# Performance work log

Measured on AMD Instinct MI355X. Metric: run time of the kernel, lower is better.

## Reference

```python
import jax, jax.numpy as jnp
import numpy as np

B, N, IN_F, OUT_F, H = 4, 2048, 128, 128, 4
D = OUT_F // H  # head_dim = 32
NEG_SLOPE = 0.2


def setup_inputs() -> dict:
    key = jax.random.key(0)
    k1, k2, k3, k4, k5 = jax.random.split(key, 5)
    x = jax.random.normal(k1, (B, N, IN_F), dtype=jnp.float32)
    adj = jax.random.randint(k2, (N, N), 0, 2, dtype=jnp.int32)
    adj = adj.at[jnp.arange(N), jnp.arange(N)].set(1)  # self-loops
    # xavier-uniform-like init
    lim_w = float(np.sqrt(6.0 / (IN_F + OUT_F)))
    W = jax.random.uniform(k3, (OUT_F, IN_F), minval=-lim_w, maxval=lim_w, dtype=jnp.float32)
    lim_a = float(np.sqrt(6.0 / (H + D)))
    a_src = jax.random.uniform(k4, (H, D), minval=-lim_a, maxval=lim_a, dtype=jnp.float32)
    a_dst = jax.random.uniform(k5, (H, D), minval=-lim_a, maxval=lim_a, dtype=jnp.float32)
    return {"x": x, "adj": adj, "W": W, "a_src": a_src, "a_dst": a_dst}


def reference(x, adj, W, a_src, a_dst):
    Bx, Nx, _ = x.shape
    # linear projection: (B,N,out) -> (B,N,H,D)
    h = jnp.einsum('bni,oi->bno', x, W).reshape(Bx, Nx, H, D)
    e_src = jnp.einsum('bnhd,hd->bnh', h, a_src)  # (B,N,H)
    e_dst = jnp.einsum('bnhd,hd->bnh', h, a_dst)  # (B,N,H)
    # scores: (B,N_src,H,N_dst)
    scores = jax.nn.leaky_relu(
        e_src[:, :, :, None] + e_dst.transpose(0, 2, 1)[:, None, :, :],
        negative_slope=NEG_SLOPE,
    )
    mask = adj[None, :, None, :]  # (1,N,1,N)
    scores = jnp.where(mask == 0, -jnp.inf, scores)
    attn = jax.nn.softmax(scores, axis=-1)  # (B,N,H,N); dropout is identity at eval
    out = jnp.einsum('bnhm,bmhd->bnhd', attn, h)  # (B,N,H,D)
    return out.reshape(Bx, Nx, H * D)
```

## Files before the change

### kernel.cpp

```cpp
#include <hip/hip_runtime.h>
#include <math.h>

#define BB 4
#define NN 2048
#define FF 128
#define HH 4
#define DD 32
#define NEG_SLOPE 0.2f
#define LOG2E 1.4426950408889634f

typedef __attribute__((ext_vector_type(8))) short short8;
typedef __attribute__((ext_vector_type(4))) float floatx4;
typedef __attribute__((ext_vector_type(2))) float floatx2;

__device__ __forceinline__ float exp2_fast(float x) {
#if __has_builtin(__builtin_amdgcn_exp2f)
    return __builtin_amdgcn_exp2f(x);
#else
    return exp2f(x);
#endif
}

__device__ __forceinline__ int bit_mask(unsigned int w, int bit) {
#if __has_builtin(__builtin_amdgcn_sbfe)
    return __builtin_amdgcn_sbfe((int)w, bit, 1);
#else
    return ((int)(w << (31 - bit))) >> 31;
#endif
}

__device__ __forceinline__ unsigned short to_bf16(float f) {
    unsigned int ui = __float_as_uint(f);
    ui += 0x7FFFu + ((ui >> 16) & 1u);
    return (unsigned short)(ui >> 16);
}

__global__ __launch_bounds__(256) void k_prep(const float* __restrict__ x,
                                              const float* __restrict__ W,
                                              const float* __restrict__ a_src,
                                              const float* __restrict__ a_dst,
                                              const int* __restrict__ adj,
                                              unsigned short* __restrict__ ht,
                                              float* __restrict__ es_t,
                                              float* __restrict__ ed_t,
                                              unsigned int* __restrict__ bits) {
    __shared__ float xs[16][FF];
    __shared__ float wt[32][132];
    __shared__ float as_s[FF], ad_s[FF];
    __shared__ unsigned short tile2[16][136];
    int t = threadIdx.x;

    if (blockIdx.x >= 512) {
        int idx = (blockIdx.x - 512) * 256 + t;
        int n = idx >> 6, w = idx & 63;
        const int4* base = (const int4*)(adj + (size_t)n * NN + w * 32);
        unsigned int word = 0;
#pragma unroll
        for (int q = 0; q < 8; ++q) {
            int4 a = base[q];
            word |= ((unsigned int)(a.x & 1)) << (q * 4 + 0);
            word |= ((unsigned int)(a.y & 1)) << (q * 4 + 1);
            word |= ((unsigned int)(a.z & 1)) << (q * 4 + 2);
            word |= ((unsigned int)(a.w & 1)) << (q * 4 + 3);
        }
        bits[idx] = word;
        return;
    }

    long rows0 = (long)blockIdx.x * 16;
    if (t < FF) { as_s[t] = a_src[t]; ad_s[t] = a_dst[t]; }
#pragma unroll
    for (int k = 0; k < 2; ++k) {
        int q = t + k * 256;
        int r = q >> 5, c4 = q & 31;
        float4 v = ((const float4*)(x + (rows0 + r) * FF))[c4];
        *(float4*)&xs[r][c4 * 4] = v;
    }
    int og = t & 31, rg = t >> 5;
    float acc[2][4];
#pragma unroll
    for (int a = 0; a < 2; ++a)
#pragma unroll
        for (int c = 0; c < 4; ++c) acc[a][c] = 0.f;

    int wo = t & 127, wg = t >> 7;
    for (int i0 = 0; i0 < FF; i0 += 32) {
        __syncthreads();
#pragma unroll
        for (int u = 0; u < 4; ++u) {
            float4 v = *(const float4*)(W + (long)wo * FF + i0 + wg * 16 + u * 4);
            wt[wg * 16 + u * 4 + 0][wo] = v.x;
            wt[wg * 16 + u * 4 + 1][wo] = v.y;
            wt[wg * 16 + u * 4 + 2][wo] = v.z;
            wt[wg * 16 + u * 4 + 3][wo] = v.w;
        }
        __syncthreads();
#pragma unroll
        for (int i = 0; i < 32; ++i) {
            float4 w4 = *(const float4*)&wt[i][og * 4];
            float x0 = xs[rg * 2 + 0][i0 + i];
            float x1 = xs[rg * 2 + 1][i0 + i];
            acc[0][0] += x0 * w4.x; acc[0][1] += x0 * w4.y;
            acc[0][2] += x0 * w4.z; acc[0][3] += x0 * w4.w;
            acc[1][0] += x1 * w4.x; acc[1][1] += x1 * w4.y;
            acc[1][2] += x1 * w4.z; acc[1][3] += x1 * w4.w;
        }
    }

    int head = og >> 3;
    int b = (int)(rows0 >> 11);
    int m_block = (int)(rows0 & 2047);
    float es0 = 0.f, ed0 = 0.f, es1 = 0.f, ed1 = 0.f;
#pragma unroll
    for (int c = 0; c < 4; ++c) {
        int col = og * 4 + c;
        es0 += acc[0][c] * as_s[col]; ed0 += acc[0][c] * ad_s[col];
        es1 += acc[1][c] * as_s[col]; ed1 += acc[1][c] * ad_s[col];
    }
#pragma unroll
    for (int k = 1; k < 8; k <<= 1) {
        es0 += __shfl_xor(es0, k); ed0 += __shfl_xor(ed0, k);
        es1 += __shfl_xor(es1, k); ed1 += __shfl_xor(ed1, k);
    }
    if ((og & 7) == 0) {
        size_t eb = (size_t)(b * HH + head) * NN + m_block + rg * 2;
        es_t[eb]     = es0 * LOG2E; ed_t[eb]     = ed0 * LOG2E;
        es_t[eb + 1] = es1 * LOG2E; ed_t[eb + 1] = ed1 * LOG2E;
    }

#pragma unroll
    for (int a = 0; a < 2; ++a)
#pragma unroll
        for (int c = 0; c < 4; ++c)
            tile2[rg * 2 + a][og * 4 + c] = to_bf16(acc[a][c]);
    __syncthreads();
    {
        int cg = t >> 1, half = t & 1;
        int d = cg & 31, hd = cg >> 5;
        unsigned short tmp[8];
#pragma unroll
        for (int j = 0; j < 8; ++j) tmp[j] = tile2[half * 8 + j][cg];
        unsigned short* op = ht + ((size_t)(b * HH + hd) * DD + d) * NN + m_block + half * 8;
        *(int4*)op = *(const int4*)tmp;
    }
}

#define HTS 2056
__global__ __launch_bounds__(1024) void k_attn(
        const unsigned short* __restrict__ ht,
        const unsigned int* __restrict__ bits,
        const float* __restrict__ es_t,
        const float* __restrict__ ed_t,
        float* __restrict__ out) {
    __shared__ unsigned short hb[DD * HTS];
    __shared__ float ep[NN * 2];
    int t = threadIdx.x;
    int n0 = blockIdx.x * 128;
    int bh = blockIdx.y;
    int b = bh >> 2, head = bh & 3;

    int wid = t >> 6, lane = t & 63;
    int q = lane >> 4, r = lane & 15;
    int qo = q * 8;
    int half = wid >> 3, wsub = wid & 7;
    int n_l = wsub * 16 + r;

    {
        float2 v = ((const float2*)(ed_t + (size_t)bh * NN))[t];
        float4 o;
        o.x = exp2_fast(v.x); o.y = exp2_fast(NEG_SLOPE * v.x);
        o.z = exp2_fast(v.y); o.w = exp2_fast(NEG_SLOPE * v.y);
        ((float4*)ep)[t] = o;
    }
    {
        const unsigned short* htp = ht + (size_t)bh * DD * NN;
#pragma unroll
        for (int k = 0; k < 8; ++k) {
            int qq = t + k * 1024;
            int d = qq >> 8, cm = qq & 255;
            int4 v = *(const int4*)(htp + (size_t)d * NN + cm * 8);
            *(int4*)&hb[d * HTS + cm * 8] = v;
        }
    }
    int4 bw[8];
    {
        const int4* bp = (const int4*)(bits + (size_t)(n0 + n_l) * 64 + half * 32);
#pragma unroll
        for (int g = 0; g < 8; ++g) bw[g] = bp[g];
    }
    float esv = es_t[(size_t)bh * NN + n0 + n_l];
    floatx2 es2 = {exp2_fast(esv), exp2_fast(NEG_SLOPE * esv)};
    __syncthreads();

    floatx4 acc0 = {0.f, 0.f, 0.f, 0.f};
    floatx4 acc1 = {0.f, 0.f, 0.f, 0.f};
    floatx4 accd = {0.f, 0.f, 0.f, 0.f};
    union { short8 s8; int i[4]; } ones;
    ones.i[0] = 0x3F803F80; ones.i[1] = 0x3F803F80;
    ones.i[2] = 0x3F803F80; ones.i[3] = 0x3F803F80;

    const float* eph = ep + half * 2048;
    const unsigned short* hrow0 = &hb[r * HTS + half * 1024 + qo];
    const unsigned short* hrow1 = hrow0 + 16 * HTS;

#pragma unroll
    for (int g = 0; g < 8; ++g) {
#pragma unroll
        for (int c = 0; c < 4; ++c) {
            unsigned int word = (unsigned int)((&bw[g].x)[c]);
            int mb = (g * 4 + c) * 32;
            unsigned int wq = word >> qo;
            const float* pbase = eph + (mb + qo) * 2;
            union { short8 s8; int i[4]; } af;
#pragma unroll
            for (int jp = 0; jp < 4; ++jp) {
                float4 d2 = *(const float4*)(pbase + jp * 4);
                floatx2 p0 = es2 * (floatx2){d2.x, d2.y};
                floatx2 p1 = es2 * (floatx2){d2.z, d2.w};
                float w0 = fmaxf(p0.x, p0.y);
                float w1 = fmaxf(p1.x, p1.y);
                int m0 = bit_mask(wq, 2 * jp);
                int m1 = bit_mask(wq, 2 * jp + 1);
                w0 = __uint_as_float(__float_as_uint(w0) & (unsigned int)m0);
                w1 = __uint_as_float(__float_as_uint(w1) & (unsigned int)m1);
                af.i[jp] = __builtin_amdgcn_perm(__float_as_uint(w1),
                                                 __float_as_uint(w0),
                                                 0x07060302u);
            }
            short8 b0 = *(const short8*)(hrow0 + mb);
            short8 b1 = *(const short8*)(hrow1 + mb);
            acc0 = __builtin_amdgcn_mfma_f32_16x16x32_bf16(af.s8, b0, acc0, 0, 0, 0);
            acc1 = __builtin_amdgcn_mfma_f32_16x16x32_bf16(af.s8, b1, acc1, 0, 0, 0);
            accd = __builtin_amdgcn_mfma_f32_16x16x32_bf16(af.s8, ones.s8, accd, 0, 0, 0);
        }
    }

    __syncthreads();
    float* scr = (float*)hb;
    if (wid >= 8) {
        int base = ((wid - 8) * 64 + lane) * 12;
        *(floatx4*)&scr[base + 0] = acc0;
        *(floatx4*)&scr[base + 4] = acc1;
        *(floatx4*)&scr[base + 8] = accd;
    }
    __syncthreads();
    if (wid < 8) {
        int base = (wid * 64 + lane) * 12;
        floatx4 p0 = *(const floatx4*)&scr[base + 0];
        floatx4 p1 = *(const floatx4*)&scr[base + 4];
        floatx4 pd = *(const floatx4*)&scr[base + 8];
#pragma unroll
        for (int k = 0; k < 4; ++k) {
            acc0[k] += p0[k]; acc1[k] += p1[k]; accd[k] += pd[k];
        }
#pragma unroll
        for (int reg = 0; reg < 4; ++reg) {
            int nrow = n0 + wsub * 16 + q * 4 + reg;
            float inv = 1.0f / accd[reg];
            float* op = out + ((size_t)(b * NN + nrow)) * FF + head * DD;
            op[r]      = acc0[reg] * inv;
            op[16 + r] = acc1[reg] * inv;
        }
    }
}

extern "C" void kernel_launch(void* const* d_in, const int* in_sizes, int n_in,
                              void* d_out, int out_size, void* d_ws, size_t ws_size,
                              hipStream_t stream) {
    const float* x     = (const float*)d_in[0];
    const int*   adj   = (const int*)d_in[1];
    const float* W     = (const float*)d_in[2];
    const float* a_src = (const float*)d_in[3];
    const float* a_dst = (const float*)d_in[4];
    float* out = (float*)d_out;

    float* es_t = (float*)d_ws;
    float* ed_t = es_t + (size_t)BB * HH * NN;
    unsigned int* bits = (unsigned int*)(ed_t + (size_t)BB * HH * NN);
    unsigned short* ht = (unsigned short*)(bits + (size_t)NN * (NN / 32));

    hipLaunchKernelGGL(k_prep, dim3(1024), dim3(256), 0, stream,
                       x, W, a_src, a_dst, adj, ht, es_t, ed_t, bits);
    hipLaunchKernelGGL(k_attn, dim3(NN / 128, BB * HH), dim3(1024), 0, stream,
                       ht, bits, es_t, ed_t, out);
}
```

Measured before the change: 102.5 us.

## Restructure prep GEMM tiling and halve attention block with packed bf16 exp tables

The prep kernel drops to 128 threads per block, each computing a 4x4 output tile with float4 dot products over a row-major W tile, and the bitmask blocks are regridded to match. The attention kernel uses 64-row blocks of 512 threads and stages h in two 1024-column halves to cut shared memory, which should raise occupancy. It also stores the destination exp pair as packed bf16 in one uint instead of two floats. The cost is an extra barrier-separated load phase and reduced precision in the exponent factors.

```diff
diff --git a/kernel.cpp b/kernel.cpp
--- a/kernel.cpp
+++ b/kernel.cpp
@@ -35,7 +35,13 @@
     return (unsigned short)(ui >> 16);
 }
 
-__global__ __launch_bounds__(256) void k_prep(const float* __restrict__ x,
+__device__ __forceinline__ unsigned int pack_pair(float e) {
+    unsigned int p = to_bf16(exp2_fast(e));
+    unsigned int n = to_bf16(exp2_fast(NEG_SLOPE * e));
+    return (p << 16) | n;
+}
+
+__global__ __launch_bounds__(128) void k_prep(const float* __restrict__ x,
                                               const float* __restrict__ W,
                                               const float* __restrict__ a_src,
                                               const float* __restrict__ a_dst,
@@ -44,14 +50,14 @@
                                               float* __restrict__ es_t,
                                               float* __restrict__ ed_t,
                                               unsigned int* __restrict__ bits) {
-    __shared__ float xs[16][FF];
-    __shared__ float wt[32][132];
+    __shared__ float xs[16][132];
+    __shared__ float wb[128][36];
     __shared__ float as_s[FF], ad_s[FF];
     __shared__ unsigned short tile2[16][136];
     int t = threadIdx.x;
 
     if (blockIdx.x >= 512) {
-        int idx = (blockIdx.x - 512) * 256 + t;
+        int idx = (blockIdx.x - 512) * 128 + t;
         int n = idx >> 6, w = idx & 63;
         const int4* base = (const int4*)(adj + (size_t)n * NN + w * 32);
         unsigned int word = 0;
@@ -68,129 +74,137 @@
     }
 
     long rows0 = (long)blockIdx.x * 16;
-    if (t < FF) { as_s[t] = a_src[t]; ad_s[t] = a_dst[t]; }
-#pragma unroll
-    for (int k = 0; k < 2; ++k) {
-        int q = t + k * 256;
-        int r = q >> 5, c4 = q & 31;
-        float4 v = ((const float4*)(x + (rows0 + r) * FF))[c4];
-        *(float4*)&xs[r][c4 * 4] = v;
+    as_s[t] = a_src[t]; ad_s[t] = a_dst[t];
+#pragma unroll
+    for (int k = 0; k < 4; ++k) {
+        int idx = t + k * 128;
+        int r = idx >> 5, f4 = idx & 31;
+        float4 v = ((const float4*)(x + (rows0 + r) * FF))[f4];
+        *(float4*)&xs[r][f4 * 4] = v;
     }
     int og = t & 31, rg = t >> 5;
-    float acc[2][4];
-#pragma unroll
-    for (int a = 0; a < 2; ++a)
+    float acc[4][4];
+#pragma unroll
+    for (int a = 0; a < 4; ++a)
 #pragma unroll
         for (int c = 0; c < 4; ++c) acc[a][c] = 0.f;
 
-    int wo = t & 127, wg = t >> 7;
-    for (int i0 = 0; i0 < FF; i0 += 32) {
+    for (int c4 = 0; c4 < 4; ++c4) {
         __syncthreads();
 #pragma unroll
-        for (int u = 0; u < 4; ++u) {
-            float4 v = *(const float4*)(W + (long)wo * FF + i0 + wg * 16 + u * 4);
-            wt[wg * 16 + u * 4 + 0][wo] = v.x;
-            wt[wg * 16 + u * 4 + 1][wo] = v.y;
-            wt[wg * 16 + u * 4 + 2][wo] = v.z;
-            wt[wg * 16 + u * 4 + 3][wo] = v.w;
+        for (int k = 0; k < 8; ++k) {
+            int idx = t + k * 128;
+            int wr = idx >> 3, f4 = idx & 7;
+            float4 v = *(const float4*)(W + (long)wr * FF + c4 * 32 + f4 * 4);
+            *(float4*)&wb[wr][f4 * 4] = v;
         }
         __syncthreads();
 #pragma unroll
-        for (int i = 0; i < 32; ++i) {
-            float4 w4 = *(const float4*)&wt[i][og * 4];
-            float x0 = xs[rg * 2 + 0][i0 + i];
-            float x1 = xs[rg * 2 + 1][i0 + i];
-            acc[0][0] += x0 * w4.x; acc[0][1] += x0 * w4.y;
-            acc[0][2] += x0 * w4.z; acc[0][3] += x0 * w4.w;
-            acc[1][0] += x1 * w4.x; acc[1][1] += x1 * w4.y;
-            acc[1][2] += x1 * w4.z; acc[1][3] += x1 * w4.w;
+        for (int ii = 0; ii < 8; ++ii) {
+            int i = ii * 4;
+            float4 xv[4], wv[4];
+#pragma unroll
+            for (int a = 0; a < 4; ++a)
+                xv[a] = *(const float4*)&xs[rg * 4 + a][c4 * 32 + i];
+#pragma unroll
+            for (int c = 0; c < 4; ++c)
+                wv[c] = *(const float4*)&wb[og * 4 + c][i];
+#pragma unroll
+            for (int a = 0; a < 4; ++a)
+#pragma unroll
+                for (int c = 0; c < 4; ++c) {
+                    acc[a][c] += xv[a].x * wv[c].x + xv[a].y * wv[c].y
+                               + xv[a].z * wv[c].z + xv[a].w * wv[c].w;
+                }
         }
     }
 
     int head = og >> 3;
     int b = (int)(rows0 >> 11);
     int m_block = (int)(rows0 & 2047);
-    float es0 = 0.f, ed0 = 0.f, es1 = 0.f, ed1 = 0.f;
-#pragma unroll
-    for (int c = 0; c < 4; ++c) {
-        int col = og * 4 + c;
-        es0 += acc[0][c] * as_s[col]; ed0 += acc[0][c] * ad_s[col];
-        es1 += acc[1][c] * as_s[col]; ed1 += acc[1][c] * ad_s[col];
+    float es[4], ed[4];
+#pragma unroll
+    for (int a = 0; a < 4; ++a) {
+        float s = 0.f, d = 0.f;
+#pragma unroll
+        for (int c = 0; c < 4; ++c) {
+            int col = og * 4 + c;
+            s += acc[a][c] * as_s[col];
+            d += acc[a][c] * ad_s[col];
+        }
+        es[a] = s; ed[a] = d;
     }
 #pragma unroll
     for (int k = 1; k < 8; k <<= 1) {
-        es0 += __shfl_xor(es0, k); ed0 += __shfl_xor(ed0, k);
-        es1 += __shfl_xor(es1, k); ed1 += __shfl_xor(ed1, k);
+#pragma unroll
+        for (int a = 0; a < 4; ++a) {
+            es[a] += __shfl_xor(es[a], k);
+            ed[a] += __shfl_xor(ed[a], k);
+        }
     }
     if ((og & 7) == 0) {
-        size_t eb = (size_t)(b * HH + head) * NN + m_block + rg * 2;
-        es_t[eb]     = es0 * LOG2E; ed_t[eb]     = ed0 * LOG2E;
-        es_t[eb + 1] = es1 * LOG2E; ed_t[eb + 1] = ed1 * LOG2E;
-    }
-
-#pragma unroll
-    for (int a = 0; a < 2; ++a)
+        size_t eb = (size_t)(b * HH + head) * NN + m_block + rg * 4;
+#pragma unroll
+        for (int a = 0; a < 4; ++a) {
+            es_t[eb + a] = es[a] * LOG2E;
+            ed_t[eb + a] = ed[a] * LOG2E;
+        }
+    }
+
+#pragma unroll
+    for (int a = 0; a < 4; ++a)
 #pragma unroll
         for (int c = 0; c < 4; ++c)
-            tile2[rg * 2 + a][og * 4 + c] = to_bf16(acc[a][c]);
+            tile2[rg * 4 + a][og * 4 + c] = to_bf16(acc[a][c]);
     __syncthreads();
     {
-        int cg = t >> 1, half = t & 1;
-        int d = cg & 31, hd = cg >> 5;
-        unsigned short tmp[8];
-#pragma unroll
-        for (int j = 0; j < 8; ++j) tmp[j] = tile2[half * 8 + j][cg];
-        unsigned short* op = ht + ((size_t)(b * HH + hd) * DD + d) * NN + m_block + half * 8;
-        *(int4*)op = *(const int4*)tmp;
-    }
-}
-
-#define HTS 2056
-__global__ __launch_bounds__(1024) void k_attn(
+        int col = t;
+        int hd = col >> 5, d = col & 31;
+        unsigned short* op = ht + ((size_t)(b * HH + hd) * DD + d) * NN + m_block;
+#pragma unroll
+        for (int h2 = 0; h2 < 2; ++h2) {
+            unsigned short tmp[8];
+#pragma unroll
+            for (int j = 0; j < 8; ++j) tmp[j] = tile2[h2 * 8 + j][col];
+            *(int4*)(op + h2 * 8) = *(const int4*)tmp;
+        }
+    }
+}
+
+#define HBS 1032
+__global__ __launch_bounds__(512) void k_attn(
         const unsigned short* __restrict__ ht,
         const unsigned int* __restrict__ bits,
         const float* __restrict__ es_t,
         const float* __restrict__ ed_t,
         float* __restrict__ out) {
-    __shared__ unsigned short hb[DD * HTS];
-    __shared__ float ep[NN * 2];
+    __shared__ unsigned short hb[DD * HBS];
+    __shared__ unsigned int epk[NN];
     int t = threadIdx.x;
-    int n0 = blockIdx.x * 128;
+    int n0 = blockIdx.x * 64;
     int bh = blockIdx.y;
     int b = bh >> 2, head = bh & 3;
 
     int wid = t >> 6, lane = t & 63;
     int q = lane >> 4, r = lane & 15;
     int qo = q * 8;
-    int half = wid >> 3, wsub = wid & 7;
-    int n_l = wsub * 16 + r;
+    int ks = wid >> 2, rg2 = wid & 3;
+    int n_row = n0 + rg2 * 16 + r;
 
     {
-        float2 v = ((const float2*)(ed_t + (size_t)bh * NN))[t];
-        float4 o;
-        o.x = exp2_fast(v.x); o.y = exp2_fast(NEG_SLOPE * v.x);
-        o.z = exp2_fast(v.y); o.w = exp2_fast(NEG_SLOPE * v.y);
-        ((float4*)ep)[t] = o;
-    }
-    {
-        const unsigned short* htp = ht + (size_t)bh * DD * NN;
-#pragma unroll
-        for (int k = 0; k < 8; ++k) {
-            int qq = t + k * 1024;
-            int d = qq >> 8, cm = qq & 255;
-            int4 v = *(const int4*)(htp + (size_t)d * NN + cm * 8);
-            *(int4*)&hb[d * HTS + cm * 8] = v;
-        }
+        float4 v = ((const float4*)(ed_t + (size_t)bh * NN))[t];
+        uint4 o = {pack_pair(v.x), pack_pair(v.y), pack_pair(v.z), pack_pair(v.w)};
+        ((uint4*)epk)[t] = o;
     }
     int4 bw[8];
     {
-        const int4* bp = (const int4*)(bits + (size_t)(n0 + n_l) * 64 + half * 32);
-#pragma unroll
-        for (int g = 0; g < 8; ++g) bw[g] = bp[g];
-    }
-    float esv = es_t[(size_t)bh * NN + n0 + n_l];
+        const int4* bp0 = (const int4*)(bits + (size_t)n_row * 64 + ks * 16);
+        const int4* bp1 = (const int4*)(bits + (size_t)n_row * 64 + 32 + ks * 16);
+#pragma unroll
+        for (int g = 0; g < 4; ++g) { bw[g] = bp0[g]; bw[4 + g] = bp1[g]; }
+    }
+    float esv = es_t[(size_t)bh * NN + n_row];
     floatx2 es2 = {exp2_fast(esv), exp2_fast(NEG_SLOPE * esv)};
-    __syncthreads();
 
     floatx4 acc0 = {0.f, 0.f, 0.f, 0.f};
     floatx4 acc1 = {0.f, 0.f, 0.f, 0.f};
@@ -199,24 +213,41 @@
     ones.i[0] = 0x3F803F80; ones.i[1] = 0x3F803F80;
     ones.i[2] = 0x3F803F80; ones.i[3] = 0x3F803F80;
 
-    const float* eph = ep + half * 2048;
-    const unsigned short* hrow0 = &hb[r * HTS + half * 1024 + qo];
-    const unsigned short* hrow1 = hrow0 + 16 * HTS;
-
-#pragma unroll
-    for (int g = 0; g < 8; ++g) {
-#pragma unroll
-        for (int c = 0; c < 4; ++c) {
-            unsigned int word = (unsigned int)((&bw[g].x)[c]);
-            int mb = (g * 4 + c) * 32;
+    const unsigned short* htp = ht + (size_t)bh * DD * NN;
+
+    for (int half = 0; half < 2; ++half) {
+        __syncthreads();
+#pragma unroll
+        for (int k = 0; k < 8; ++k) {
+            int qq = t + k * 512;
+            int d = qq >> 7, cm = qq & 127;
+            int4 v = *(const int4*)(htp + (size_t)d * NN + half * 1024 + cm * 8);
+            *(int4*)&hb[d * HBS + cm * 8] = v;
+        }
+        __syncthreads();
+        const unsigned int* pq = epk + half * 1024 + ks * 512;
+        const unsigned short* h0 = &hb[r * HBS + ks * 512 + qo];
+        const unsigned short* h1 = &hb[(16 + r) * HBS + ks * 512 + qo];
+        int bbase = half * 4;
+
+#pragma unroll
+        for (int it = 0; it < 16; ++it) {
+            unsigned int word = (unsigned int)((&bw[bbase + (it >> 2)].x)[it & 3]);
+            int mb = it * 32;
             unsigned int wq = word >> qo;
-            const float* pbase = eph + (mb + qo) * 2;
+            uint4 u0 = *(const uint4*)(pq + mb + qo);
+            uint4 u1 = *(const uint4*)(pq + mb + qo + 4);
             union { short8 s8; int i[4]; } af;
 #pragma unroll
             for (int jp = 0; jp < 4; ++jp) {
-                float4 d2 = *(const float4*)(pbase + jp * 4);
-                floatx2 p0 = es2 * (floatx2){d2.x, d2.y};
-                floatx2 p1 = es2 * (floatx2){d2.z, d2.w};
+                unsigned int c0 = (jp < 2) ? (&u0.x)[jp * 2]     : (&u1.x)[(jp - 2) * 2];
+                unsigned int c1 = (jp < 2) ? (&u0.x)[jp * 2 + 1] : (&u1.x)[(jp - 2) * 2 + 1];
+                floatx2 d0 = {__uint_as_float(c0 & 0xFFFF0000u),
+                              __uint_as_float(c0 << 16)};
+                floatx2 d1 = {__uint_as_float(c1 & 0xFFFF0000u),
+                              __uint_as_float(c1 << 16)};
+                floatx2 p0 = es2 * d0;
+                floatx2 p1 = es2 * d1;
                 float w0 = fmaxf(p0.x, p0.y);
                 float w1 = fmaxf(p1.x, p1.y);
                 int m0 = bit_mask(wq, 2 * jp);
@@ -227,8 +258,8 @@
                                                  __float_as_uint(w0),
                                                  0x07060302u);
             }
-            short8 b0 = *(const short8*)(hrow0 + mb);
-            short8 b1 = *(const short8*)(hrow1 + mb);
+            short8 b0 = *(const short8*)(h0 + mb);
+            short8 b1 = *(const short8*)(h1 + mb);
             acc0 = __builtin_amdgcn_mfma_f32_16x16x32_bf16(af.s8, b0, acc0, 0, 0, 0);
             acc1 = __builtin_amdgcn_mfma_f32_16x16x32_bf16(af.s8, b1, acc1, 0, 0, 0);
             accd = __builtin_amdgcn_mfma_f32_16x16x32_bf16(af.s8, ones.s8, accd, 0, 0, 0);
@@ -237,15 +268,15 @@
 
     __syncthreads();
     float* scr = (float*)hb;
-    if (wid >= 8) {
-        int base = ((wid - 8) * 64 + lane) * 12;
+    if (ks == 1) {
+        int base = (rg2 * 64 + lane) * 12;
         *(floatx4*)&scr[base + 0] = acc0;
         *(floatx4*)&scr[base + 4] = acc1;
         *(floatx4*)&scr[base + 8] = accd;
     }
     __syncthreads();
-    if (wid < 8) {
-        int base = (wid * 64 + lane) * 12;
+    if (ks == 0) {
+        int base = (rg2 * 64 + lane) * 12;
         floatx4 p0 = *(const floatx4*)&scr[base + 0];
         floatx4 p1 = *(const floatx4*)&scr[base + 4];
         floatx4 pd = *(const floatx4*)&scr[base + 8];
@@ -255,7 +286,7 @@
         }
 #pragma unroll
         for (int reg = 0; reg < 4; ++reg) {
-            int nrow = n0 + wsub * 16 + q * 4 + reg;
+            int nrow = n0 + rg2 * 16 + q * 4 + reg;
             float inv = 1.0f / accd[reg];
             float* op = out + ((size_t)(b * NN + nrow)) * FF + head * DD;
             op[r]      = acc0[reg] * inv;
@@ -279,8 +310,8 @@
     unsigned int* bits = (unsigned int*)(ed_t + (size_t)BB * HH * NN);
     unsigned short* ht = (unsigned short*)(bits + (size_t)NN * (NN / 32));
 
-    hipLaunchKernelGGL(k_prep, dim3(1024), dim3(256), 0, stream,
+    hipLaunchKernelGGL(k_prep, dim3(1536), dim3(128), 0, stream,
                        x, W, a_src, a_dst, adj, ht, es_t, ed_t, bits);
-    hipLaunchKernelGGL(k_attn, dim3(NN / 128, BB * HH), dim3(1024), 0, stream,
+    hipLaunchKernelGGL(k_attn, dim3(NN / 64, BB * HH), dim3(512), 0, stream,
                        ht, bits, es_t, ed_t, out);
 }
```

Measured after the change: 116.5 us. 13.6% more time.
